# Kernel tuning notes

Hardware: AMD Instinct MI355X
Metric: run time of the kernel (lower is better)

The kernel has to match this reference:

```python
import jax, jax.numpy as jnp
import numpy as np

ND = 56          # descriptor length
NATOMS = 50000   # total atoms across all configs
NCONF = 100      # number of configurations
APC = NATOMS // NCONF  # atoms per config
NEI = 20         # avg neighbors per atom
M = NATOMS * NEI * 3   # derivative rows (x/y/z interleaved)
H = 64           # hidden width


def _net(x, W1, b1, W2, b2, W3, b3):
    # Small MLP energy model: [N, ND] -> [N, 1]
    h = jax.nn.silu(x @ W1 + b1)
    h = jax.nn.silu(h @ W2 + b2)
    return h @ W3 + b3


def setup_inputs() -> dict:
    key = jax.random.key(0)
    ks = jax.random.split(key, 12)
    x = jax.random.normal(ks[0], (NATOMS, ND), jnp.float32)
    xd = jax.random.normal(ks[1], (M, ND), jnp.float32)
    # atom i belongs to config i // APC (sorted, consistent with atoms_per_structure)
    indices = (jnp.arange(NATOMS) // APC).astype(jnp.int32)
    atoms_per_structure = jnp.full((NCONF,), APC, dtype=jnp.int32)
    # xd_indx: col0 = atom i whose descriptor derivative this row holds,
    #          col1 = unused neighbor tag, col2 = cartesian coord in {0,1,2}
    col0 = jax.random.randint(ks[2], (M,), 0, NATOMS, dtype=jnp.int32)
    col1 = jnp.zeros((M,), jnp.int32)
    col2 = jnp.tile(jnp.arange(3, dtype=jnp.int32), M // 3)
    xd_indx = jnp.stack([col0, col1, col2], axis=1)
    unique_j = jax.random.randint(ks[3], (M,), 0, NATOMS, dtype=jnp.int32)
    # MLP parameters
    W1 = jax.random.normal(ks[4], (ND, H), jnp.float32) / np.sqrt(ND)
    b1 = jnp.zeros((H,), jnp.float32)
    W2 = jax.random.normal(ks[5], (H, H), jnp.float32) / np.sqrt(H)
    b2 = jnp.zeros((H,), jnp.float32)
    W3 = jax.random.normal(ks[6], (H, 1), jnp.float32) / np.sqrt(H)
    b3 = jnp.zeros((1,), jnp.float32)
    return {"x": x, "xd": xd, "indices": indices,
            "atoms_per_structure": atoms_per_structure,
            "xd_indx": xd_indx, "unique_j": unique_j,
            "W1": W1, "b1": b1, "W2": W2, "b2": b2, "W3": W3, "b3": b3}


def reference(x, xd, indices, atoms_per_structure, xd_indx, unique_j,
              W1, b1, W2, b2, W3, b3):
    natoms = x.shape[0]
    nconf = atoms_per_structure.shape[0]

    # --- energy path: per-atom energies scattered to per-config totals ---
    per_atom_e = _net(x, W1, b1, W2, b2, W3, b3)[:, 0]           # [natoms]
    predicted_energy_total = jax.ops.segment_sum(
        per_atom_e, indices, num_segments=nconf)                  # [nconf]

    # --- force path: dE/dD gather, elementwise mul with dD/dR, scatter ---
    def total_e(xx):
        return jnp.sum(_net(xx, W1, b1, W2, b2, W3, b3))
    dEdD = jax.grad(total_e)(x)                                   # [natoms, ND]

    # Gather dEdD rows per derivative entry, contract over descriptor dim.
    # (equivalent to the per-coordinate masked mul + index_add + sum in torch)
    vals = jnp.sum(xd * dEdD[xd_indx[:, 0]], axis=1)              # [M]
    # flattened (atom j, coord) target index: j*3 + coord -> matches
    # torch.flatten(cat([fx, fy, fz], dim=1)) layout
    seg = unique_j * 3 + xd_indx[:, 2]                            # [M]
    predicted_forces = jax.ops.segment_sum(
        vals, seg, num_segments=3 * natoms)                       # [3*natoms]

    return (predicted_energy_total, predicted_forces)
```

## Files before the change

kernel.cpp:

```cpp
#include <hip/hip_runtime.h>
#include <hip/hip_fp16.h>

#define ND 56
#define HD 64
#define S1 60
#define S2 68
#define DEDD_H2 32
#define ESUM_MAX 1024
#define FBLK 2048

typedef float v4f __attribute__((ext_vector_type(4)));
typedef _Float16 v4h __attribute__((ext_vector_type(4)));

__global__ __launch_bounds__(256) void zero_kernel(float* __restrict__ p, int n) {
    int i = blockIdx.x * 256 + threadIdx.x;
    if (i < n) p[i] = 0.f;
}

__global__ __launch_bounds__(256) void mlp_kernel(
    const float* __restrict__ x, const int* __restrict__ indices,
    const float* __restrict__ W1, const float* __restrict__ b1,
    const float* __restrict__ W2, const float* __restrict__ b2,
    const float* __restrict__ W3, const float* __restrict__ b3,
    float* __restrict__ e_out, __half2* __restrict__ dEdD,
    int natoms, int nconf)
{
    __shared__ float W1T[HD * S1 + 4];
    __shared__ float W2T[HD * S2];
    __shared__ float b1s[HD], b2s[HD], W3s[HD];
    __shared__ float xs[16 * ND];
    __shared__ float hbuf[4][4][HD];
    __shared__ float gbuf[4][4][HD];
    __shared__ float esum[ESUM_MAX];

    const int tid = threadIdx.x;
    for (int i = tid; i < ND * HD; i += 256) W1T[(i % HD) * S1 + (i / HD)] = W1[i];
    for (int i = tid; i < HD * HD; i += 256) W2T[(i % HD) * S2 + (i / HD)] = W2[i];
    for (int i = tid; i < ESUM_MAX; i += 256) esum[i] = 0.f;
    if (tid < HD) { b1s[tid] = b1[tid]; b2s[tid] = b2[tid]; W3s[tid] = W3[tid]; }
    __syncthreads();

    const int w = tid >> 6, lane = tid & 63;
    const float b3v = b3[0];
    const float b1v = b1s[lane], b2v = b2s[lane], w3v = W3s[lane];
    const int nGroups = (natoms + 15) >> 4;
    const bool ldsE = (nconf <= ESUM_MAX);

    for (int grp = blockIdx.x; grp < nGroups; grp += gridDim.x) {
        const int abase = grp * 16 + w * 4;

        if (lane < 56) {
            const int a = lane / 14;
            if (abase + a < natoms)
                reinterpret_cast<float4*>(xs + w * 4 * ND)[lane] =
                    reinterpret_cast<const float4*>(x)[(size_t)abase * 14 + lane];
        }

        float4 acc[4];
        #pragma unroll
        for (int a = 0; a < 4; ++a) acc[a] = float4{0.f, 0.f, 0.f, 0.f};
        #pragma unroll
        for (int i = 0; i < 14; ++i) {
            const float4 wv = *reinterpret_cast<const float4*>(&W1T[lane * S1 + 4 * i]);
            #pragma unroll
            for (int a = 0; a < 4; ++a) {
                const float4 xv = *reinterpret_cast<const float4*>(&xs[(w * 4 + a) * ND + 4 * i]);
                acc[a].x = fmaf(wv.x, xv.x, acc[a].x);
                acc[a].y = fmaf(wv.y, xv.y, acc[a].y);
                acc[a].z = fmaf(wv.z, xv.z, acc[a].z);
                acc[a].w = fmaf(wv.w, xv.w, acc[a].w);
            }
        }
        float z1[4], s1[4];
        #pragma unroll
        for (int a = 0; a < 4; ++a) {
            z1[a] = b1v + ((acc[a].x + acc[a].y) + (acc[a].z + acc[a].w));
            s1[a] = 1.f / (1.f + __expf(-z1[a]));
            hbuf[w][a][lane] = z1[a] * s1[a];
        }

        #pragma unroll
        for (int a = 0; a < 4; ++a) acc[a] = float4{0.f, 0.f, 0.f, 0.f};
        #pragma unroll
        for (int i = 0; i < 16; ++i) {
            const float4 wv = *reinterpret_cast<const float4*>(&W2T[lane * S2 + 4 * i]);
            #pragma unroll
            for (int a = 0; a < 4; ++a) {
                const float4 hv = *reinterpret_cast<const float4*>(&hbuf[w][a][4 * i]);
                acc[a].x = fmaf(wv.x, hv.x, acc[a].x);
                acc[a].y = fmaf(wv.y, hv.y, acc[a].y);
                acc[a].z = fmaf(wv.z, hv.z, acc[a].z);
                acc[a].w = fmaf(wv.w, hv.w, acc[a].w);
            }
        }
        float ev[4];
        #pragma unroll
        for (int a = 0; a < 4; ++a) {
            const float z2 = b2v + ((acc[a].x + acc[a].y) + (acc[a].z + acc[a].w));
            const float s2 = 1.f / (1.f + __expf(-z2));
            ev[a] = (z2 * s2) * w3v;
            gbuf[w][a][lane] = w3v * (s2 * (1.f + z2 * (1.f - s2)));
        }
        #pragma unroll
        for (int off = 32; off > 0; off >>= 1) {
            #pragma unroll
            for (int a = 0; a < 4; ++a) ev[a] += __shfl_xor(ev[a], off);
        }
        if (lane == 0) {
            #pragma unroll
            for (int a = 0; a < 4; ++a)
                if (abase + a < natoms) {
                    const int conf = indices[abase + a];
                    if (ldsE) atomicAdd(&esum[conf], ev[a] + b3v);
                    else      unsafeAtomicAdd(&e_out[conf], ev[a] + b3v);
                }
        }

        #pragma unroll
        for (int a = 0; a < 4; ++a) acc[a] = float4{0.f, 0.f, 0.f, 0.f};
        #pragma unroll
        for (int i = 0; i < 16; ++i) {
            const float w0 = W2T[(4 * i + 0) * S2 + lane];
            const float w1v = W2T[(4 * i + 1) * S2 + lane];
            const float w2v = W2T[(4 * i + 2) * S2 + lane];
            const float w3x = W2T[(4 * i + 3) * S2 + lane];
            #pragma unroll
            for (int a = 0; a < 4; ++a) {
                const float4 gv = *reinterpret_cast<const float4*>(&gbuf[w][a][4 * i]);
                acc[a].x = fmaf(w0, gv.x, acc[a].x);
                acc[a].y = fmaf(w1v, gv.y, acc[a].y);
                acc[a].z = fmaf(w2v, gv.z, acc[a].z);
                acc[a].w = fmaf(w3x, gv.w, acc[a].w);
            }
        }
        #pragma unroll
        for (int a = 0; a < 4; ++a) {
            const float dh1 = (acc[a].x + acc[a].y) + (acc[a].z + acc[a].w);
            hbuf[w][a][lane] = dh1 * (s1[a] * (1.f + z1[a] * (1.f - s1[a])));
        }

        #pragma unroll
        for (int a = 0; a < 4; ++a) acc[a] = float4{0.f, 0.f, 0.f, 0.f};
        #pragma unroll
        for (int i = 0; i < 16; ++i) {
            const float w0 = W1T[(4 * i + 0) * S1 + lane];
            const float w1v = W1T[(4 * i + 1) * S1 + lane];
            const float w2v = W1T[(4 * i + 2) * S1 + lane];
            const float w3x = W1T[(4 * i + 3) * S1 + lane];
            #pragma unroll
            for (int a = 0; a < 4; ++a) {
                const float4 gv = *reinterpret_cast<const float4*>(&hbuf[w][a][4 * i]);
                acc[a].x = fmaf(w0, gv.x, acc[a].x);
                acc[a].y = fmaf(w1v, gv.y, acc[a].y);
                acc[a].z = fmaf(w2v, gv.z, acc[a].z);
                acc[a].w = fmaf(w3x, gv.w, acc[a].w);
            }
        }
        #pragma unroll
        for (int a = 0; a < 4; ++a) {
            const float v  = (acc[a].x + acc[a].y) + (acc[a].z + acc[a].w);
            const float vh = __shfl_down(v, 1);
            if ((lane & 1) == 0 && lane < ND && abase + a < natoms)
                dEdD[(size_t)(abase + a) * DEDD_H2 + (lane >> 1)] =
                    __floats2half2_rn(v, vh);
        }
    }

    if (ldsE) {
        __syncthreads();
        for (int c = tid; c < nconf; c += 256) {
            const float v = esum[c];
            if (v != 0.f) unsafeAtomicAdd(&e_out[c], v);
        }
    }
}

__global__ __launch_bounds__(256) void force_kernel(
    const float* __restrict__ xd,
    const int*   __restrict__ xd_indx,
    const int*   __restrict__ unique_j,
    const _Float16* __restrict__ dEdD,
    float* __restrict__ out_f,
    int M, int CH)
{
    const int b = blockIdx.x, tid = threadIdx.x;
    const int team = tid >> 4, sub = tid & 15;
    const int mstart = b * CH;
    const int mend   = min(mstart + CH, M);

    for (int m0 = mstart; m0 < mend; m0 += 16) {
        const int m = m0 + team;
        float partial = 0.f;
        const bool act = (m < mend);
        if (act && sub < 14) {
            const int a = __builtin_nontemporal_load(xd_indx + 3 * (size_t)m);
            const v4f u = __builtin_nontemporal_load(
                reinterpret_cast<const v4f*>(xd) + (size_t)m * 14 + sub);
            const v4h hv = reinterpret_cast<const v4h*>(dEdD + ((size_t)a << 6))[sub];
            partial = fmaf(u.x, (float)hv.x,
                      fmaf(u.y, (float)hv.y,
                      fmaf(u.z, (float)hv.z, u.w * (float)hv.w)));
        }
        partial += __shfl_xor(partial, 1);
        partial += __shfl_xor(partial, 2);
        partial += __shfl_xor(partial, 4);
        partial += __shfl_xor(partial, 8);

        if (act && sub == 0) {
            const int coord = __builtin_nontemporal_load(xd_indx + 3 * (size_t)m + 2);
            const int j     = __builtin_nontemporal_load(unique_j + m);
            unsafeAtomicAdd(&out_f[(size_t)j * 3 + coord], partial);
        }
    }
}

extern "C" void kernel_launch(void* const* d_in, const int* in_sizes, int n_in,
                              void* d_out, int out_size, void* d_ws, size_t ws_size,
                              hipStream_t stream) {
    const float* x        = (const float*)d_in[0];
    const float* xd       = (const float*)d_in[1];
    const int*   indices  = (const int*)d_in[2];
    const int*   xd_indx  = (const int*)d_in[4];
    const int*   unique_j = (const int*)d_in[5];
    const float* W1 = (const float*)d_in[6];
    const float* b1 = (const float*)d_in[7];
    const float* W2 = (const float*)d_in[8];
    const float* b2 = (const float*)d_in[9];
    const float* W3 = (const float*)d_in[10];
    const float* b3 = (const float*)d_in[11];

    const int natoms = in_sizes[0] / ND;
    const int M      = in_sizes[1] / ND;
    const int nconf  = in_sizes[3];

    float*    out_e = (float*)d_out;
    float*    out_f = out_e + nconf;
    __half2*  dEdD2 = (__half2*)d_ws;
    _Float16* dEdDh = (_Float16*)d_ws;

    zero_kernel<<<(out_size + 255) / 256, 256, 0, stream>>>((float*)d_out, out_size);

    const int nGroups = (natoms + 15) >> 4;
    const int mlpGrid = nGroups < 768 ? nGroups : 768;
    mlp_kernel<<<mlpGrid, 256, 0, stream>>>(
        x, indices, W1, b1, W2, b2, W3, b3, out_e, dEdD2, natoms, nconf);

    const int CH = (M + FBLK - 1) / FBLK;
    force_kernel<<<FBLK, 256, 0, stream>>>(
        xd, xd_indx, unique_j, dEdDh, out_f, M, CH);
}
```

Before: 325.1 us.

## Software-pipeline force kernel with double-buffered 4-row batches per team

Each 16-lane team now processes 4 derivative rows per step instead of one, and the kernel alternates between two register batches so the loads for the next 64 rows are issued before the current batch is reduced and atomically scattered. The aim is to keep more memory requests in flight and hide the latency of the streaming xd reads and the random dEdD gathers. The per-block chunk is rounded up to a multiple of 128 rows, which changes the grid size slightly. The cost is higher register use per thread, which may lower occupancy.

```diff
diff --git a/kernel.cpp b/kernel.cpp
--- a/kernel.cpp
+++ b/kernel.cpp
@@ -175,6 +175,57 @@
     }
 }
 
+struct FBatch {
+    v4f uu[4];
+    v4h hh[4];
+    int cc[4];
+    int jj[4];
+};
+
+__device__ __forceinline__ void fload(
+    FBatch& B, int m0, int team, int sub, int mend,
+    const float* __restrict__ xd, const int* __restrict__ xd_indx,
+    const int* __restrict__ unique_j, const _Float16* __restrict__ dEdD)
+{
+    #pragma unroll
+    for (int r = 0; r < 4; ++r) {
+        const int m = m0 + 4 * team + r;
+        if (m < mend) {
+            if (sub < 14) {
+                const int a = __builtin_nontemporal_load(xd_indx + 3 * (size_t)m);
+                B.uu[r] = __builtin_nontemporal_load(
+                    reinterpret_cast<const v4f*>(xd) + (size_t)m * 14 + sub);
+                B.hh[r] = reinterpret_cast<const v4h*>(dEdD + ((size_t)a << 6))[sub];
+            }
+            if (sub == 0) {
+                B.cc[r] = __builtin_nontemporal_load(xd_indx + 3 * (size_t)m + 2);
+                B.jj[r] = __builtin_nontemporal_load(unique_j + m);
+            }
+        }
+    }
+}
+
+__device__ __forceinline__ void fcompat(
+    const FBatch& B, int m0, int team, int sub, int mend,
+    float* __restrict__ out_f)
+{
+    #pragma unroll
+    for (int r = 0; r < 4; ++r) {
+        const int m = m0 + 4 * team + r;
+        float p = 0.f;
+        if (m < mend && sub < 14)
+            p = fmaf(B.uu[r].x, (float)B.hh[r].x,
+                fmaf(B.uu[r].y, (float)B.hh[r].y,
+                fmaf(B.uu[r].z, (float)B.hh[r].z, B.uu[r].w * (float)B.hh[r].w)));
+        p += __shfl_xor(p, 1);
+        p += __shfl_xor(p, 2);
+        p += __shfl_xor(p, 4);
+        p += __shfl_xor(p, 8);
+        if (m < mend && sub == 0)
+            unsafeAtomicAdd(&out_f[(size_t)B.jj[r] * 3 + B.cc[r]], p);
+    }
+}
+
 __global__ __launch_bounds__(256) void force_kernel(
     const float* __restrict__ xd,
     const int*   __restrict__ xd_indx,
@@ -187,30 +238,18 @@
     const int team = tid >> 4, sub = tid & 15;
     const int mstart = b * CH;
     const int mend   = min(mstart + CH, M);
-
-    for (int m0 = mstart; m0 < mend; m0 += 16) {
-        const int m = m0 + team;
-        float partial = 0.f;
-        const bool act = (m < mend);
-        if (act && sub < 14) {
-            const int a = __builtin_nontemporal_load(xd_indx + 3 * (size_t)m);
-            const v4f u = __builtin_nontemporal_load(
-                reinterpret_cast<const v4f*>(xd) + (size_t)m * 14 + sub);
-            const v4h hv = reinterpret_cast<const v4h*>(dEdD + ((size_t)a << 6))[sub];
-            partial = fmaf(u.x, (float)hv.x,
-                      fmaf(u.y, (float)hv.y,
-                      fmaf(u.z, (float)hv.z, u.w * (float)hv.w)));
-        }
-        partial += __shfl_xor(partial, 1);
-        partial += __shfl_xor(partial, 2);
-        partial += __shfl_xor(partial, 4);
-        partial += __shfl_xor(partial, 8);
-
-        if (act && sub == 0) {
-            const int coord = __builtin_nontemporal_load(xd_indx + 3 * (size_t)m + 2);
-            const int j     = __builtin_nontemporal_load(unique_j + m);
-            unsafeAtomicAdd(&out_f[(size_t)j * 3 + coord], partial);
-        }
+    if (mstart >= mend) return;
+
+    FBatch A = {}, B = {};
+
+    fload(A, mstart, team, sub, mend, xd, xd_indx, unique_j, dEdD);
+    for (int m0 = mstart; m0 < mend; m0 += 128) {
+        const int m1 = m0 + 64;
+        if (m1 < mend) fload(B, m1, team, sub, mend, xd, xd_indx, unique_j, dEdD);
+        fcompat(A, m0, team, sub, mend, out_f);
+        const int m2 = m0 + 128;
+        if (m2 < mend) fload(A, m2, team, sub, mend, xd, xd_indx, unique_j, dEdD);
+        if (m1 < mend) fcompat(B, m1, team, sub, mend, out_f);
     }
 }
 
@@ -245,7 +284,9 @@
     mlp_kernel<<<mlpGrid, 256, 0, stream>>>(
         x, indices, W1, b1, W2, b2, W3, b3, out_e, dEdD2, natoms, nconf);
 
-    const int CH = (M + FBLK - 1) / FBLK;
-    force_kernel<<<FBLK, 256, 0, stream>>>(
+    int CH = (M + FBLK - 1) / FBLK;
+    CH = (CH + 127) & ~127;
+    const int fGrid = (M + CH - 1) / CH;
+    force_kernel<<<fGrid, 256, 0, stream>>>(
         xd, xd_indx, unique_j, dEdDh, out_f, M, CH);
 }
```

Result: slower. 429.2 us (+32.0%).

## Run MLP forward and backward passes on MFMA fp16 matrix instructions

Applied to the files above, without the earlier changes.

Replaces the scalar-FMA MLP kernel with one where each wavefront processes 16 atoms. The forward passes, the backward passes through W2 and W1, and the dE/dD output all use 16x16x32 fp16 MFMA instructions. Weights are pre-laid-out in LDS as MFMA B fragments and held in registers, and activations are staged per wave in fp16 LDS rows. The goal is to cut ALU and LDS traffic in the MLP stage. The cost is lower input and intermediate precision, because x and activations are now rounded to fp16. The grid is fixed at 512 blocks with a launch-bounds occupancy hint, and the LDS energy accumulator is shrunk.

```diff
diff --git a/kernel.cpp b/kernel.cpp
--- a/kernel.cpp
+++ b/kernel.cpp
@@ -3,171 +3,231 @@
 
 #define ND 56
 #define HD 64
-#define S1 60
-#define S2 68
 #define DEDD_H2 32
-#define ESUM_MAX 1024
+#define ESUM_MAX 512
 #define FBLK 2048
+#define XROW 72
 
 typedef float v4f __attribute__((ext_vector_type(4)));
 typedef _Float16 v4h __attribute__((ext_vector_type(4)));
+typedef _Float16 half8 __attribute__((ext_vector_type(8)));
+typedef float f32x4 __attribute__((ext_vector_type(4)));
+
+__device__ __forceinline__ unsigned pk2h(float a, float b) {
+    unsigned short ha = __builtin_bit_cast(unsigned short, (_Float16)a);
+    unsigned short hb = __builtin_bit_cast(unsigned short, (_Float16)b);
+    return (unsigned)ha | ((unsigned)hb << 16);
+}
 
 __global__ __launch_bounds__(256) void zero_kernel(float* __restrict__ p, int n) {
     int i = blockIdx.x * 256 + threadIdx.x;
     if (i < n) p[i] = 0.f;
 }
 
-__global__ __launch_bounds__(256) void mlp_kernel(
+__global__ __launch_bounds__(256, 2) void mlp_kernel(
     const float* __restrict__ x, const int* __restrict__ indices,
     const float* __restrict__ W1, const float* __restrict__ b1,
     const float* __restrict__ W2, const float* __restrict__ b2,
     const float* __restrict__ W3, const float* __restrict__ b3,
-    float* __restrict__ e_out, __half2* __restrict__ dEdD,
+    float* __restrict__ e_out, _Float16* __restrict__ dEdD,
     int natoms, int nconf)
 {
-    __shared__ float W1T[HD * S1 + 4];
-    __shared__ float W2T[HD * S2];
-    __shared__ float b1s[HD], b2s[HD], W3s[HD];
-    __shared__ float xs[16 * ND];
-    __shared__ float hbuf[4][4][HD];
-    __shared__ float gbuf[4][4][HD];
+    __shared__ _Float16 wfrag[4][4096];
+    __shared__ _Float16 xh[4][16 * XROW];
     __shared__ float esum[ESUM_MAX];
 
     const int tid = threadIdx.x;
-    for (int i = tid; i < ND * HD; i += 256) W1T[(i % HD) * S1 + (i / HD)] = W1[i];
-    for (int i = tid; i < HD * HD; i += 256) W2T[(i % HD) * S2 + (i / HD)] = W2[i];
+    for (int idx = tid; idx < 4 * 4096; idx += 256) {
+        const int mat = idx >> 12;
+        const int r   = idx & 4095;
+        const int j  = r & 7;
+        const int ln = (r >> 3) & 63;
+        const int nt = (r >> 9) & 3;
+        const int ks = r >> 11;
+        const int k = ks * 32 + (ln >> 4) * 8 + j;
+        const int n = nt * 16 + (ln & 15);
+        float v;
+        if (mat == 0)      v = (k < ND) ? W1[k * HD + n] : 0.f;
+        else if (mat == 1) v = W2[k * HD + n];
+        else if (mat == 2) v = W2[n * HD + k];
+        else               v = (n < ND) ? W1[n * HD + k] : 0.f;
+        wfrag[mat][r] = (_Float16)v;
+    }
     for (int i = tid; i < ESUM_MAX; i += 256) esum[i] = 0.f;
-    if (tid < HD) { b1s[tid] = b1[tid]; b2s[tid] = b2[tid]; W3s[tid] = W3[tid]; }
     __syncthreads();
 
     const int w = tid >> 6, lane = tid & 63;
+    const int col = lane & 15, g = lane >> 4;
+
+    half8 wb[4][2][4];
+    #pragma unroll
+    for (int mat = 0; mat < 4; ++mat)
+        #pragma unroll
+        for (int ks = 0; ks < 2; ++ks)
+            #pragma unroll
+            for (int t = 0; t < 4; ++t)
+                wb[mat][ks][t] = *reinterpret_cast<const half8*>(
+                    &wfrag[mat][((ks * 4 + t) * 64 + lane) * 8]);
+
+    float b1v[4], b2v[4], w3v[4];
+    #pragma unroll
+    for (int t = 0; t < 4; ++t) {
+        b1v[t] = b1[t * 16 + col];
+        b2v[t] = b2[t * 16 + col];
+        w3v[t] = W3[t * 16 + col];
+    }
     const float b3v = b3[0];
-    const float b1v = b1s[lane], b2v = b2s[lane], w3v = W3s[lane];
+    const bool ldsE = (nconf <= ESUM_MAX);
+
+    _Float16* xw = &xh[w][0];
     const int nGroups = (natoms + 15) >> 4;
-    const bool ldsE = (nconf <= ESUM_MAX);
-
-    for (int grp = blockIdx.x; grp < nGroups; grp += gridDim.x) {
-        const int abase = grp * 16 + w * 4;
-
-        if (lane < 56) {
-            const int a = lane / 14;
-            if (abase + a < natoms)
-                reinterpret_cast<float4*>(xs + w * 4 * ND)[lane] =
-                    reinterpret_cast<const float4*>(x)[(size_t)abase * 14 + lane];
-        }
-
-        float4 acc[4];
-        #pragma unroll
-        for (int a = 0; a < 4; ++a) acc[a] = float4{0.f, 0.f, 0.f, 0.f};
-        #pragma unroll
-        for (int i = 0; i < 14; ++i) {
-            const float4 wv = *reinterpret_cast<const float4*>(&W1T[lane * S1 + 4 * i]);
-            #pragma unroll
-            for (int a = 0; a < 4; ++a) {
-                const float4 xv = *reinterpret_cast<const float4*>(&xs[(w * 4 + a) * ND + 4 * i]);
-                acc[a].x = fmaf(wv.x, xv.x, acc[a].x);
-                acc[a].y = fmaf(wv.y, xv.y, acc[a].y);
-                acc[a].z = fmaf(wv.z, xv.z, acc[a].z);
-                acc[a].w = fmaf(wv.w, xv.w, acc[a].w);
-            }
-        }
-        float z1[4], s1[4];
-        #pragma unroll
-        for (int a = 0; a < 4; ++a) {
-            z1[a] = b1v + ((acc[a].x + acc[a].y) + (acc[a].z + acc[a].w));
-            s1[a] = 1.f / (1.f + __expf(-z1[a]));
-            hbuf[w][a][lane] = z1[a] * s1[a];
-        }
-
-        #pragma unroll
-        for (int a = 0; a < 4; ++a) acc[a] = float4{0.f, 0.f, 0.f, 0.f};
-        #pragma unroll
-        for (int i = 0; i < 16; ++i) {
-            const float4 wv = *reinterpret_cast<const float4*>(&W2T[lane * S2 + 4 * i]);
-            #pragma unroll
-            for (int a = 0; a < 4; ++a) {
-                const float4 hv = *reinterpret_cast<const float4*>(&hbuf[w][a][4 * i]);
-                acc[a].x = fmaf(wv.x, hv.x, acc[a].x);
-                acc[a].y = fmaf(wv.y, hv.y, acc[a].y);
-                acc[a].z = fmaf(wv.z, hv.z, acc[a].z);
-                acc[a].w = fmaf(wv.w, hv.w, acc[a].w);
-            }
-        }
-        float ev[4];
-        #pragma unroll
-        for (int a = 0; a < 4; ++a) {
-            const float z2 = b2v + ((acc[a].x + acc[a].y) + (acc[a].z + acc[a].w));
-            const float s2 = 1.f / (1.f + __expf(-z2));
-            ev[a] = (z2 * s2) * w3v;
-            gbuf[w][a][lane] = w3v * (s2 * (1.f + z2 * (1.f - s2)));
-        }
-        #pragma unroll
-        for (int off = 32; off > 0; off >>= 1) {
-            #pragma unroll
-            for (int a = 0; a < 4; ++a) ev[a] += __shfl_xor(ev[a], off);
-        }
-        if (lane == 0) {
-            #pragma unroll
-            for (int a = 0; a < 4; ++a)
-                if (abase + a < natoms) {
-                    const int conf = indices[abase + a];
-                    if (ldsE) atomicAdd(&esum[conf], ev[a] + b3v);
-                    else      unsafeAtomicAdd(&e_out[conf], ev[a] + b3v);
+
+    for (int grp = blockIdx.x * 4 + w; grp < nGroups; grp += gridDim.x * 4) {
+        const int abase = grp * 16;
+
+        #pragma unroll
+        for (int c = 0; c < 4; ++c) {
+            const int v = lane * 4 + c * 256;
+            const int atom = v >> 6, d = v & 63;
+            unsigned long long u = 0ull;
+            if (d < ND && abase + atom < natoms) {
+                const v4f xv = *reinterpret_cast<const v4f*>(
+                    &x[(size_t)(abase + atom) * ND + d]);
+                u = (unsigned long long)pk2h(xv.x, xv.y)
+                  | ((unsigned long long)pk2h(xv.z, xv.w) << 32);
+            }
+            *reinterpret_cast<unsigned long long*>(&xw[atom * XROW + d]) = u;
+        }
+
+        f32x4 z1[4];
+        #pragma unroll
+        for (int t = 0; t < 4; ++t) z1[t] = f32x4{b1v[t], b1v[t], b1v[t], b1v[t]};
+        #pragma unroll
+        for (int ks = 0; ks < 2; ++ks) {
+            const half8 a = *reinterpret_cast<const half8*>(
+                &xw[col * XROW + g * 8 + ks * 32]);
+            #pragma unroll
+            for (int t = 0; t < 4; ++t)
+                z1[t] = __builtin_amdgcn_mfma_f32_16x16x32_f16(a, wb[0][ks][t], z1[t], 0, 0, 0);
+        }
+        #pragma unroll
+        for (int t = 0; t < 4; ++t)
+            #pragma unroll
+            for (int i = 0; i < 4; ++i) {
+                const float z = z1[t][i];
+                const float h = z / (1.f + __expf(-z));
+                const float hn = __shfl_xor(h, 1);
+                if ((lane & 1) == 0)
+                    *reinterpret_cast<unsigned*>(
+                        &xw[(4 * g + i) * XROW + t * 16 + col]) = pk2h(h, hn);
+            }
+
+        f32x4 z2[4];
+        #pragma unroll
+        for (int t = 0; t < 4; ++t) z2[t] = f32x4{b2v[t], b2v[t], b2v[t], b2v[t]};
+        #pragma unroll
+        for (int ks = 0; ks < 2; ++ks) {
+            const half8 a = *reinterpret_cast<const half8*>(
+                &xw[col * XROW + g * 8 + ks * 32]);
+            #pragma unroll
+            for (int t = 0; t < 4; ++t)
+                z2[t] = __builtin_amdgcn_mfma_f32_16x16x32_f16(a, wb[1][ks][t], z2[t], 0, 0, 0);
+        }
+        float e0 = 0.f, e1 = 0.f, e2 = 0.f, e3 = 0.f;
+        #pragma unroll
+        for (int t = 0; t < 4; ++t)
+            #pragma unroll
+            for (int i = 0; i < 4; ++i) {
+                const float z = z2[t][i];
+                const float s = 1.f / (1.f + __expf(-z));
+                const float h2 = z * s;
+                const float ec = h2 * w3v[t];
+                if (i == 0) e0 += ec; else if (i == 1) e1 += ec;
+                else if (i == 2) e2 += ec; else e3 += ec;
+                const float gv = w3v[t] * (s * (1.f + z * (1.f - s)));
+                const float gn = __shfl_xor(gv, 1);
+                if ((lane & 1) == 0)
+                    *reinterpret_cast<unsigned*>(
+                        &xw[(4 * g + i) * XROW + t * 16 + col]) = pk2h(gv, gn);
+            }
+        float e[4] = {e0, e1, e2, e3};
+        #pragma unroll
+        for (int i = 0; i < 4; ++i) {
+            e[i] += __shfl_xor(e[i], 1);
+            e[i] += __shfl_xor(e[i], 2);
+            e[i] += __shfl_xor(e[i], 4);
+            e[i] += __shfl_xor(e[i], 8);
+        }
+        if (col == 0) {
+            #pragma unroll
+            for (int i = 0; i < 4; ++i) {
+                const int atom = abase + 4 * g + i;
+                if (atom < natoms) {
+                    const int conf = indices[atom];
+                    if (ldsE) atomicAdd(&esum[conf], e[i] + b3v);
+                    else      unsafeAtomicAdd(&e_out[conf], e[i] + b3v);
                 }
-        }
-
-        #pragma unroll
-        for (int a = 0; a < 4; ++a) acc[a] = float4{0.f, 0.f, 0.f, 0.f};
-        #pragma unroll
-        for (int i = 0; i < 16; ++i) {
-            const float w0 = W2T[(4 * i + 0) * S2 + lane];
-            const float w1v = W2T[(4 * i + 1) * S2 + lane];
-            const float w2v = W2T[(4 * i + 2) * S2 + lane];
-            const float w3x = W2T[(4 * i + 3) * S2 + lane];
-            #pragma unroll
-            for (int a = 0; a < 4; ++a) {
-                const float4 gv = *reinterpret_cast<const float4*>(&gbuf[w][a][4 * i]);
-                acc[a].x = fmaf(w0, gv.x, acc[a].x);
-                acc[a].y = fmaf(w1v, gv.y, acc[a].y);
-                acc[a].z = fmaf(w2v, gv.z, acc[a].z);
-                acc[a].w = fmaf(w3x, gv.w, acc[a].w);
-            }
-        }
-        #pragma unroll
-        for (int a = 0; a < 4; ++a) {
-            const float dh1 = (acc[a].x + acc[a].y) + (acc[a].z + acc[a].w);
-            hbuf[w][a][lane] = dh1 * (s1[a] * (1.f + z1[a] * (1.f - s1[a])));
-        }
-
-        #pragma unroll
-        for (int a = 0; a < 4; ++a) acc[a] = float4{0.f, 0.f, 0.f, 0.f};
-        #pragma unroll
-        for (int i = 0; i < 16; ++i) {
-            const float w0 = W1T[(4 * i + 0) * S1 + lane];
-            const float w1v = W1T[(4 * i + 1) * S1 + lane];
-            const float w2v = W1T[(4 * i + 2) * S1 + lane];
-            const float w3x = W1T[(4 * i + 3) * S1 + lane];
-            #pragma unroll
-            for (int a = 0; a < 4; ++a) {
-                const float4 gv = *reinterpret_cast<const float4*>(&hbuf[w][a][4 * i]);
-                acc[a].x = fmaf(w0, gv.x, acc[a].x);
-                acc[a].y = fmaf(w1v, gv.y, acc[a].y);
-                acc[a].z = fmaf(w2v, gv.z, acc[a].z);
-                acc[a].w = fmaf(w3x, gv.w, acc[a].w);
-            }
-        }
-        #pragma unroll
-        for (int a = 0; a < 4; ++a) {
-            const float v  = (acc[a].x + acc[a].y) + (acc[a].z + acc[a].w);
-            const float vh = __shfl_down(v, 1);
-            if ((lane & 1) == 0 && lane < ND && abase + a < natoms)
-                dEdD[(size_t)(abase + a) * DEDD_H2 + (lane >> 1)] =
-                    __floats2half2_rn(v, vh);
-        }
-    }
-
+            }
+        }
+
+        f32x4 dh[4];
+        #pragma unroll
+        for (int t = 0; t < 4; ++t) dh[t] = f32x4{0.f, 0.f, 0.f, 0.f};
+        #pragma unroll
+        for (int ks = 0; ks < 2; ++ks) {
+            const half8 a = *reinterpret_cast<const half8*>(
+                &xw[col * XROW + g * 8 + ks * 32]);
+            #pragma unroll
+            for (int t = 0; t < 4; ++t)
+                dh[t] = __builtin_amdgcn_mfma_f32_16x16x32_f16(a, wb[2][ks][t], dh[t], 0, 0, 0);
+        }
+        #pragma unroll
+        for (int t = 0; t < 4; ++t)
+            #pragma unroll
+            for (int i = 0; i < 4; ++i) {
+                const float z = z1[t][i];
+                const float s = 1.f / (1.f + __expf(-z));
+                const float gv = dh[t][i] * (s * (1.f + z * (1.f - s)));
+                const float gn = __shfl_xor(gv, 1);
+                if ((lane & 1) == 0)
+                    *reinterpret_cast<unsigned*>(
+                        &xw[(4 * g + i) * XROW + t * 16 + col]) = pk2h(gv, gn);
+            }
+
+        f32x4 dx[4];
+        #pragma unroll
+        for (int t = 0; t < 4; ++t) dx[t] = f32x4{0.f, 0.f, 0.f, 0.f};
+        #pragma unroll
+        for (int ks = 0; ks < 2; ++ks) {
+            const half8 a = *reinterpret_cast<const half8*>(
+                &xw[col * XROW + g * 8 + ks * 32]);
+            #pragma unroll
+            for (int t = 0; t < 4; ++t)
+                dx[t] = __builtin_amdgcn_mfma_f32_16x16x32_f16(a, wb[3][ks][t], dx[t], 0, 0, 0);
+        }
+        #pragma unroll
+        for (int t = 0; t < 4; ++t)
+            #pragma unroll
+            for (int i = 0; i < 4; ++i) {
+                const float v = dx[t][i];
+                const float vn = __shfl_xor(v, 1);
+                if ((lane & 1) == 0)
+                    *reinterpret_cast<unsigned*>(
+                        &xw[(4 * g + i) * XROW + t * 16 + col]) = pk2h(v, vn);
+            }
+        #pragma unroll
+        for (int c = 0; c < 2; ++c) {
+            const int atom = lane >> 2;
+            const int seg = (lane & 3) * 2 + c;
+            const half8 vv = *reinterpret_cast<const half8*>(&xw[atom * XROW + seg * 8]);
+            if (abase + atom < natoms)
+                *reinterpret_cast<half8*>(
+                    &dEdD[(size_t)(abase + atom) * 64 + seg * 8]) = vv;
+        }
+    }
+
+    __syncthreads();
     if (ldsE) {
-        __syncthreads();
         for (int c = tid; c < nconf; c += 256) {
             const float v = esum[c];
             if (v != 0.f) unsafeAtomicAdd(&e_out[c], v);
@@ -235,15 +295,12 @@
 
     float*    out_e = (float*)d_out;
     float*    out_f = out_e + nconf;
-    __half2*  dEdD2 = (__half2*)d_ws;
     _Float16* dEdDh = (_Float16*)d_ws;
 
     zero_kernel<<<(out_size + 255) / 256, 256, 0, stream>>>((float*)d_out, out_size);
 
-    const int nGroups = (natoms + 15) >> 4;
-    const int mlpGrid = nGroups < 768 ? nGroups : 768;
-    mlp_kernel<<<mlpGrid, 256, 0, stream>>>(
-        x, indices, W1, b1, W2, b2, W3, b3, out_e, dEdD2, natoms, nconf);
+    mlp_kernel<<<512, 256, 0, stream>>>(
+        x, indices, W1, b1, W2, b2, W3, b3, out_e, dEdDh, natoms, nconf);
 
     const int CH = (M + FBLK - 1) / FBLK;
     force_kernel<<<FBLK, 256, 0, stream>>>(
```

After: 273.8 us. 15.8% less time.
